# Performance work log

Hardware: AMD Instinct MI355X
Metric: run time of the kernel (lower is better)

The kernel has to match this reference:

```python
import jax, jax.numpy as jnp
import numpy as np

NUM_NODES = 50000
NUM_REL_ORIG = 5            # original relation types
NUM_REL = 2 * NUM_REL_ORIG + 1  # augmented: original + inverse + self-loop = 11
F_IN = 128
F_OUT = 128
NUM_EDGES = 800000


def setup_inputs() -> dict:
    key = jax.random.key(0)
    k1, k2, k3, k4, k5, k6 = jax.random.split(key, 6)
    src = jax.random.randint(k1, (NUM_EDGES,), 0, NUM_NODES, dtype=jnp.int32)
    rel = jax.random.randint(k2, (NUM_EDGES,), 0, NUM_REL_ORIG, dtype=jnp.int32)
    dst = jax.random.randint(k3, (NUM_EDGES,), 0, NUM_NODES, dtype=jnp.int32)
    graph = jnp.stack([src, rel, dst], axis=1)  # [E, 3] = (head, relation, tail)
    features = jax.random.normal(k4, (NUM_NODES, F_IN), dtype=jnp.float32)
    # RGCNConv parameters (no basis/block decomposition, bias=False, root_weight=True)
    glorot = lambda k, shape: jax.random.normal(k, shape, dtype=jnp.float32) * jnp.sqrt(2.0 / (shape[-2] + shape[-1]))
    weight = glorot(k5, (NUM_REL, F_IN, F_OUT))  # per-relation weights
    root = glorot(k6, (F_IN, F_OUT))             # root (self) weight
    return {"graph": graph, "features": features, "weight": weight, "root": root}


def reference(graph, features, weight, root):
    N = features.shape[0]
    R = weight.shape[0]
    n_orig = (R - 1) // 2
    src, rel, dst = graph[:, 0], graph[:, 1], graph[:, 2]
    loop = jnp.arange(N, dtype=graph.dtype)
    # augmented edge list: original, inverse, self-loops
    full_src = jnp.concatenate([src, dst, loop])
    full_dst = jnp.concatenate([dst, src, loop])
    full_rel = jnp.concatenate([rel, rel + n_orig, jnp.full((N,), 2 * n_orig, dtype=graph.dtype)])
    # per-(relation, dst-node) mean of source features (PyG RGCNConv aggr='mean'
    # aggregates raw x_j per relation, then applies W_r to the aggregate)
    seg = full_rel * N + full_dst  # [E_full]
    msgs = features[full_src]      # [E_full, F_in] gather
    sums = jax.ops.segment_sum(msgs, seg, num_segments=R * N)           # [R*N, F_in]
    cnts = jax.ops.segment_sum(jnp.ones((seg.shape[0],), features.dtype), seg, num_segments=R * N)
    mean = sums / jnp.maximum(cnts, 1.0)[:, None]
    mean = mean.reshape(R, N, -1)  # [R, N, F_in]
    # out = sum_r mean_r @ W_r + x @ W_root
    out = jnp.einsum('rnf,rfo->no', mean, weight) + features @ root
    return out
```

## Files before the change

### kernel.cpp

```cpp
#include <hip/hip_runtime.h>
#include <hip/hip_bf16.h>

#define NN 50000
#define RO 5
#define RT 11
#define FF 128
#define EE 800000
#define NBINS (2 * RO * NN)
#define SLOTS 32
#define FEAT_BLKS ((NN * FF / 4) / 256)
#define WT_BLKS ((RT * FF * FF) / 256)

typedef unsigned short u16;
typedef unsigned int u32;
typedef __attribute__((ext_vector_type(4))) unsigned short u16x4;
typedef __attribute__((ext_vector_type(4))) unsigned int u32x4;
typedef __attribute__((ext_vector_type(8))) short bf16x8;
typedef __attribute__((ext_vector_type(4))) float f32x4;

__device__ __forceinline__ u16 f2b(float x) {
  unsigned u = __float_as_uint(x);
  return (u16)((u + 0x7fffu + ((u >> 16) & 1u)) >> 16);
}

__global__ __launch_bounds__(256) void prep_k(const float* __restrict__ f,
                                              const float* __restrict__ w,
                                              const float* __restrict__ root,
                                              u16* __restrict__ fb,
                                              u16* __restrict__ wt) {
  int b = blockIdx.x;
  if (b < FEAT_BLKS) {
    int i = b * 256 + threadIdx.x;
    float4 v = reinterpret_cast<const float4*>(f)[i];
    u16x4 o;
    o.x = f2b(v.x); o.y = f2b(v.y); o.z = f2b(v.z); o.w = f2b(v.w);
    reinterpret_cast<u16x4*>(fb)[i] = o;
  } else if (b < FEAT_BLKS + WT_BLKS) {
    int idx = (b - FEAT_BLKS) * 256 + threadIdx.x;
    int r = idx >> 14;
    int rem = idx & 16383;
    int k = rem >> 7;
    int o = rem & 127;
    float v = w[idx];
    if (r == 10) v += root[rem];
    int chunk = (k >> 3) ^ (o & 7);
    wt[(r << 14) + (o << 7) + (chunk << 3) + (k & 7)] = f2b(v);
  } else {
    if (threadIdx.x < 64) reinterpret_cast<u32*>(fb)[NN * 64 + threadIdx.x] = 0;
  }
}

__global__ __launch_bounds__(256) void fill_k(const int* __restrict__ g,
                                              int* __restrict__ cur,
                                              u16* __restrict__ eidx) {
  const int e0 = (blockIdx.x * 256 + threadIdx.x) * 2;
  if (e0 >= EE) return;
  int s0 = g[3 * e0], r0 = g[3 * e0 + 1], d0 = g[3 * e0 + 2];
  int b0f = r0 * NN + d0;
  int b0r = (r0 + RO) * NN + s0;
  int p0f = atomicAdd(&cur[b0f], 1);
  int p0r = atomicAdd(&cur[b0r], 1);
  if (p0f < SLOTS) eidx[b0f * SLOTS + p0f] = (u16)s0;
  if (p0r < SLOTS) eidx[b0r * SLOTS + p0r] = (u16)d0;
  const int e1 = e0 + 1;
  if (e1 >= EE) return;
  int s1 = g[3 * e1], r1 = g[3 * e1 + 1], d1 = g[3 * e1 + 2];
  int b1f = r1 * NN + d1;
  int b1r = (r1 + RO) * NN + s1;
  int p1f = atomicAdd(&cur[b1f], 1);
  int p1r = atomicAdd(&cur[b1r], 1);
  if (p1f < SLOTS) eidx[b1f * SLOTS + p1f] = (u16)s1;
  if (p1r < SLOTS) eidx[b1r * SLOTS + p1r] = (u16)d1;
}

#define ACC(p) { a0 += __uint_as_float((p).x << 16); a1 += __uint_as_float((p).x & 0xffff0000u); \
                 a2 += __uint_as_float((p).y << 16); a3 += __uint_as_float((p).y & 0xffff0000u); \
                 a4 += __uint_as_float((p).z << 16); a5 += __uint_as_float((p).z & 0xffff0000u); \
                 a6 += __uint_as_float((p).w << 16); a7 += __uint_as_float((p).w & 0xffff0000u); }

__global__ __launch_bounds__(256) void mean_k(const int* __restrict__ cnt,
                                              const u32* __restrict__ eidx32,
                                              const u32x4* __restrict__ fv4,
                                              u32x4* __restrict__ Mv4) {
  const int lane = threadIdx.x & 63;
  const int wv   = threadIdx.x >> 6;
  const int q    = lane >> 4;
  const int l15  = lane & 15;
  const int q16  = q << 4;
  const int seg  = blockIdx.x * 16 + wv * 4 + q;
  const int c    = min(cnt[seg], SLOTS);
  const u32 slots = eidx32[seg * 16 + l15];

  int cmax = c;
  cmax = max(cmax, __shfl_xor(cmax, 16));
  cmax = max(cmax, __shfl_xor(cmax, 32));

  float a0 = 0.f, a1 = 0.f, a2 = 0.f, a3 = 0.f, a4 = 0.f, a5 = 0.f, a6 = 0.f, a7 = 0.f;

  for (int i = 0; i < cmax; i += 4) {
    u32 w0 = __shfl(slots, q16 + (i >> 1));
    u32 w1 = __shfl(slots, q16 + (i >> 1) + 1);
    int s0 = (i     < c) ? (int)(w0 & 0xffffu) : NN;
    int s1 = (i + 1 < c) ? (int)(w0 >> 16)     : NN;
    int s2 = (i + 2 < c) ? (int)(w1 & 0xffffu) : NN;
    int s3 = (i + 3 < c) ? (int)(w1 >> 16)     : NN;
    u32x4 p0 = fv4[s0 * 16 + l15];
    u32x4 p1 = fv4[s1 * 16 + l15];
    u32x4 p2 = fv4[s2 * 16 + l15];
    u32x4 p3 = fv4[s3 * 16 + l15];
    ACC(p0); ACC(p1); ACC(p2); ACC(p3);
  }

  const float inv = (c > 0) ? 1.0f / (float)c : 0.0f;
  u32x4 o;
  o.x = (u32)f2b(a0 * inv) | ((u32)f2b(a1 * inv) << 16);
  o.y = (u32)f2b(a2 * inv) | ((u32)f2b(a3 * inv) << 16);
  o.z = (u32)f2b(a4 * inv) | ((u32)f2b(a5 * inv) << 16);
  o.w = (u32)f2b(a6 * inv) | ((u32)f2b(a7 * inv) << 16);
  Mv4[seg * 16 + l15] = o;
}

__global__ __launch_bounds__(256) void gemm2_k(const u16* __restrict__ fbf,
                                               const u16* __restrict__ M,
                                               const u16* __restrict__ wt,
                                               float* __restrict__ out) {
  __shared__ __align__(16) u16 bs[128 * 128];
  const int tid  = threadIdx.x;
  const int lane = tid & 63;
  const int wv   = tid >> 6;
  const int l15  = lane & 15;
  const int ko   = lane >> 4;
  const int row  = blockIdx.x * 64 + wv * 16 + l15;
  const int rowc = (row < NN) ? row : 0;

  f32x4 acc[8];
#pragma unroll
  for (int i = 0; i < 8; ++i) acc[i] = (f32x4){0.f, 0.f, 0.f, 0.f};

  for (int r = 0; r < RT; ++r) {
    const bf16x8* wsrc = reinterpret_cast<const bf16x8*>(wt + (r << 14));
    bf16x8* ldst = reinterpret_cast<bf16x8*>(bs);
#pragma unroll
    for (int j = 0; j < 8; ++j) ldst[tid + j * 256] = wsrc[tid + j * 256];
    __syncthreads();

    const u16* arow = (r < 10) ? (M + ((long)r * NN + rowc) * FF)
                               : (fbf + (long)rowc * FF);
#pragma unroll
    for (int kc = 0; kc < 4; ++kc) {
      bf16x8 a = *reinterpret_cast<const bf16x8*>(arow + kc * 32 + ko * 8);
#pragma unroll
      for (int cf = 0; cf < 8; ++cf) {
        const int o = cf * 16 + l15;
        bf16x8 b = *reinterpret_cast<const bf16x8*>(
            &bs[(o << 7) + (((kc * 4 + ko) ^ (l15 & 7)) << 3)]);
        acc[cf] = __builtin_amdgcn_mfma_f32_16x16x32_bf16(a, b, acc[cf], 0, 0, 0);
      }
    }
    __syncthreads();
  }

  const int rbase = blockIdx.x * 64 + wv * 16 + ko * 4;
#pragma unroll
  for (int cf = 0; cf < 8; ++cf)
#pragma unroll
    for (int q2 = 0; q2 < 4; ++q2) {
      int rd = rbase + q2;
      if (rd < NN) out[rd * FF + cf * 16 + l15] = acc[cf][q2];
    }
}

extern "C" void kernel_launch(void* const* d_in, const int* in_sizes, int n_in,
                              void* d_out, int out_size, void* d_ws, size_t ws_size,
                              hipStream_t stream) {
  const int*   graph  = (const int*)d_in[0];
  const float* feat   = (const float*)d_in[1];
  const float* weight = (const float*)d_in[2];
  const float* root   = (const float*)d_in[3];
  float* out = (float*)d_out;
  char* ws = (char*)d_ws;

  u16* fbf  = (u16*)(ws);
  u16* wt   = (u16*)(ws + 12800512);
  int* cur  = (int*)(ws + 13160960);
  u16* eidx = (u16*)(ws + 15161088);
  u16* M    = (u16*)(ws + 47161088);

  hipMemsetAsync(cur, 0, NBINS * sizeof(int), stream);
  prep_k<<<FEAT_BLKS + WT_BLKS + 1, 256, 0, stream>>>(feat, weight, root, fbf, wt);
  fill_k<<<(EE / 2 + 255) / 256, 256, 0, stream>>>(graph, cur, eidx);
  mean_k<<<NBINS / 16, 256, 0, stream>>>(cur, (const u32*)eidx,
                                         (const u32x4*)fbf, (u32x4*)M);
  gemm2_k<<<(NN + 63) / 64, 256, 0, stream>>>(fbf, M, wt, out);
}
```

Measured before the change: 316.6 us.

## Fuse per-relation mean aggregation into GEMM, dropping intermediate mean buffer

Merges the mean-aggregation kernel and the GEMM kernel into one. Each block aggregates 32 destination nodes per relation into swizzled LDS and immediately multiplies the result by that relation's weight using MFMA. Weight fragments are read straight from global memory instead of being staged in LDS. This removes the write and re-read of the 10×N×128 bf16 mean tensor and one launch. In exchange, each block has less work per weight load, and an MFMA phase follows each gather with a barrier in between. The fill kernel also switches to one edge direction per thread for more parallelism.

```diff
diff --git a/kernel.cpp b/kernel.cpp
--- a/kernel.cpp
+++ b/kernel.cpp
@@ -6,8 +6,10 @@
 #define RT 11
 #define FF 128
 #define EE 800000
+#define EE2 (2 * EE)
 #define NBINS (2 * RO * NN)
 #define SLOTS 32
+#define DPB 32
 #define FEAT_BLKS ((NN * FF / 4) / 256)
 #define WT_BLKS ((RT * FF * FF) / 256)
 
@@ -53,121 +55,164 @@
 __global__ __launch_bounds__(256) void fill_k(const int* __restrict__ g,
                                               int* __restrict__ cur,
                                               u16* __restrict__ eidx) {
-  const int e0 = (blockIdx.x * 256 + threadIdx.x) * 2;
-  if (e0 >= EE) return;
-  int s0 = g[3 * e0], r0 = g[3 * e0 + 1], d0 = g[3 * e0 + 2];
-  int b0f = r0 * NN + d0;
-  int b0r = (r0 + RO) * NN + s0;
-  int p0f = atomicAdd(&cur[b0f], 1);
-  int p0r = atomicAdd(&cur[b0r], 1);
-  if (p0f < SLOTS) eidx[b0f * SLOTS + p0f] = (u16)s0;
-  if (p0r < SLOTS) eidx[b0r * SLOTS + p0r] = (u16)d0;
-  const int e1 = e0 + 1;
-  if (e1 >= EE) return;
-  int s1 = g[3 * e1], r1 = g[3 * e1 + 1], d1 = g[3 * e1 + 2];
-  int b1f = r1 * NN + d1;
-  int b1r = (r1 + RO) * NN + s1;
-  int p1f = atomicAdd(&cur[b1f], 1);
-  int p1r = atomicAdd(&cur[b1r], 1);
-  if (p1f < SLOTS) eidx[b1f * SLOTS + p1f] = (u16)s1;
-  if (p1r < SLOTS) eidx[b1r * SLOTS + p1r] = (u16)d1;
-}
-
-#define ACC(p) { a0 += __uint_as_float((p).x << 16); a1 += __uint_as_float((p).x & 0xffff0000u); \
-                 a2 += __uint_as_float((p).y << 16); a3 += __uint_as_float((p).y & 0xffff0000u); \
-                 a4 += __uint_as_float((p).z << 16); a5 += __uint_as_float((p).z & 0xffff0000u); \
-                 a6 += __uint_as_float((p).w << 16); a7 += __uint_as_float((p).w & 0xffff0000u); }
-
-__global__ __launch_bounds__(256) void mean_k(const int* __restrict__ cnt,
-                                              const u32* __restrict__ eidx32,
-                                              const u32x4* __restrict__ fv4,
-                                              u32x4* __restrict__ Mv4) {
-  const int lane = threadIdx.x & 63;
-  const int wv   = threadIdx.x >> 6;
-  const int q    = lane >> 4;
-  const int l15  = lane & 15;
-  const int q16  = q << 4;
-  const int seg  = blockIdx.x * 16 + wv * 4 + q;
-  const int c    = min(cnt[seg], SLOTS);
-  const u32 slots = eidx32[seg * 16 + l15];
-
-  int cmax = c;
-  cmax = max(cmax, __shfl_xor(cmax, 16));
-  cmax = max(cmax, __shfl_xor(cmax, 32));
-
-  float a0 = 0.f, a1 = 0.f, a2 = 0.f, a3 = 0.f, a4 = 0.f, a5 = 0.f, a6 = 0.f, a7 = 0.f;
-
-  for (int i = 0; i < cmax; i += 4) {
-    u32 w0 = __shfl(slots, q16 + (i >> 1));
-    u32 w1 = __shfl(slots, q16 + (i >> 1) + 1);
-    int s0 = (i     < c) ? (int)(w0 & 0xffffu) : NN;
-    int s1 = (i + 1 < c) ? (int)(w0 >> 16)     : NN;
-    int s2 = (i + 2 < c) ? (int)(w1 & 0xffffu) : NN;
-    int s3 = (i + 3 < c) ? (int)(w1 >> 16)     : NN;
-    u32x4 p0 = fv4[s0 * 16 + l15];
-    u32x4 p1 = fv4[s1 * 16 + l15];
-    u32x4 p2 = fv4[s2 * 16 + l15];
-    u32x4 p3 = fv4[s3 * 16 + l15];
-    ACC(p0); ACC(p1); ACC(p2); ACC(p3);
-  }
-
-  const float inv = (c > 0) ? 1.0f / (float)c : 0.0f;
-  u32x4 o;
-  o.x = (u32)f2b(a0 * inv) | ((u32)f2b(a1 * inv) << 16);
-  o.y = (u32)f2b(a2 * inv) | ((u32)f2b(a3 * inv) << 16);
-  o.z = (u32)f2b(a4 * inv) | ((u32)f2b(a5 * inv) << 16);
-  o.w = (u32)f2b(a6 * inv) | ((u32)f2b(a7 * inv) << 16);
-  Mv4[seg * 16 + l15] = o;
-}
-
-__global__ __launch_bounds__(256) void gemm2_k(const u16* __restrict__ fbf,
-                                               const u16* __restrict__ M,
-                                               const u16* __restrict__ wt,
-                                               float* __restrict__ out) {
-  __shared__ __align__(16) u16 bs[128 * 128];
+  const int m = blockIdx.x * 256 + threadIdx.x;
+  int e, bin; u16 val;
+  if (m < EE) {
+    e = m;
+    int s = g[3 * e], r = g[3 * e + 1], d = g[3 * e + 2];
+    bin = r * NN + d; val = (u16)s;
+  } else {
+    e = m - EE;
+    int d2 = g[3 * e], r = g[3 * e + 1], s2 = g[3 * e + 2];
+    bin = (r + RO) * NN + d2; val = (u16)s2;
+  }
+  int pos = atomicAdd(&cur[bin], 1);
+  if (pos < SLOTS) eidx[bin * SLOTS + pos] = val;
+}
+
+#define ACCX(p) { a0 += __uint_as_float((p).x << 16); a1 += __uint_as_float((p).x & 0xffff0000u); \
+                  a2 += __uint_as_float((p).y << 16); a3 += __uint_as_float((p).y & 0xffff0000u); \
+                  a4 += __uint_as_float((p).z << 16); a5 += __uint_as_float((p).z & 0xffff0000u); \
+                  a6 += __uint_as_float((p).w << 16); a7 += __uint_as_float((p).w & 0xffff0000u); }
+#define ACCY(p) { b0 += __uint_as_float((p).x << 16); b1 += __uint_as_float((p).x & 0xffff0000u); \
+                  b2 += __uint_as_float((p).y << 16); b3 += __uint_as_float((p).y & 0xffff0000u); \
+                  b4 += __uint_as_float((p).z << 16); b5 += __uint_as_float((p).z & 0xffff0000u); \
+                  b6 += __uint_as_float((p).w << 16); b7 += __uint_as_float((p).w & 0xffff0000u); }
+
+__global__ __launch_bounds__(256) void mg_k(const int* __restrict__ cnt,
+                                            const u32* __restrict__ eidx32,
+                                            const u32x4* __restrict__ fv4,
+                                            const u16* __restrict__ fbf,
+                                            const u16* __restrict__ wt,
+                                            float* __restrict__ out) {
+  __shared__ __align__(16) u32x4 Asw[DPB * 16];
   const int tid  = threadIdx.x;
   const int lane = tid & 63;
   const int wv   = tid >> 6;
   const int l15  = lane & 15;
   const int ko   = lane >> 4;
-  const int row  = blockIdx.x * 64 + wv * 16 + l15;
-  const int rowc = (row < NN) ? row : 0;
-
-  f32x4 acc[8];
-#pragma unroll
-  for (int i = 0; i < 8; ++i) acc[i] = (f32x4){0.f, 0.f, 0.f, 0.f};
-
-  for (int r = 0; r < RT; ++r) {
-    const bf16x8* wsrc = reinterpret_cast<const bf16x8*>(wt + (r << 14));
-    bf16x8* ldst = reinterpret_cast<bf16x8*>(bs);
-#pragma unroll
-    for (int j = 0; j < 8; ++j) ldst[tid + j * 256] = wsrc[tid + j * 256];
+  const int qid  = wv * 4 + ko;
+  const int q16  = ko << 4;
+  const int base = blockIdx.x * DPB;
+
+  f32x4 acc[2][2];
+#pragma unroll
+  for (int i = 0; i < 2; ++i)
+#pragma unroll
+    for (int j = 0; j < 2; ++j) acc[i][j] = (f32x4){0.f, 0.f, 0.f, 0.f};
+
+  const int row0 = qid * 2, row1 = row0 + 1;
+  const int d0 = base + row0, d1 = base + row1;
+  const bool v0 = d0 < NN, v1 = d1 < NN;
+
+  for (int r = 0; r < 10; ++r) {
+    const int seg0 = v0 ? r * NN + d0 : 0;
+    const int seg1 = v1 ? r * NN + d1 : 0;
+    const int c0 = v0 ? min(cnt[seg0], SLOTS) : 0;
+    const int c1 = v1 ? min(cnt[seg1], SLOTS) : 0;
+    const u32 sl0 = eidx32[seg0 * 16 + l15];
+    const u32 sl1 = eidx32[seg1 * 16 + l15];
+    int cmax = max(c0, c1);
+    cmax = max(cmax, __shfl_xor(cmax, 16));
+    cmax = max(cmax, __shfl_xor(cmax, 32));
+
+    float a0 = 0.f, a1 = 0.f, a2 = 0.f, a3 = 0.f, a4 = 0.f, a5 = 0.f, a6 = 0.f, a7 = 0.f;
+    float b0 = 0.f, b1 = 0.f, b2 = 0.f, b3 = 0.f, b4 = 0.f, b5 = 0.f, b6 = 0.f, b7 = 0.f;
+
+    for (int i = 0; i < cmax; i += 4) {
+      u32 wa0 = __shfl(sl0, q16 + (i >> 1));
+      u32 wa1 = __shfl(sl0, q16 + (i >> 1) + 1);
+      u32 wb0 = __shfl(sl1, q16 + (i >> 1));
+      u32 wb1 = __shfl(sl1, q16 + (i >> 1) + 1);
+      int s0 = (i     < c0) ? (int)(wa0 & 0xffffu) : NN;
+      int s1 = (i + 1 < c0) ? (int)(wa0 >> 16)     : NN;
+      int s2 = (i + 2 < c0) ? (int)(wa1 & 0xffffu) : NN;
+      int s3 = (i + 3 < c0) ? (int)(wa1 >> 16)     : NN;
+      int t0 = (i     < c1) ? (int)(wb0 & 0xffffu) : NN;
+      int t1 = (i + 1 < c1) ? (int)(wb0 >> 16)     : NN;
+      int t2 = (i + 2 < c1) ? (int)(wb1 & 0xffffu) : NN;
+      int t3 = (i + 3 < c1) ? (int)(wb1 >> 16)     : NN;
+      u32x4 p0 = fv4[s0 * 16 + l15];
+      u32x4 p1 = fv4[s1 * 16 + l15];
+      u32x4 p2 = fv4[s2 * 16 + l15];
+      u32x4 p3 = fv4[s3 * 16 + l15];
+      u32x4 p4 = fv4[t0 * 16 + l15];
+      u32x4 p5 = fv4[t1 * 16 + l15];
+      u32x4 p6 = fv4[t2 * 16 + l15];
+      u32x4 p7 = fv4[t3 * 16 + l15];
+      ACCX(p0); ACCX(p1); ACCX(p2); ACCX(p3);
+      ACCY(p4); ACCY(p5); ACCY(p6); ACCY(p7);
+    }
+
+    const float i0 = (c0 > 0) ? 1.0f / (float)c0 : 0.0f;
+    const float i1 = (c1 > 0) ? 1.0f / (float)c1 : 0.0f;
+    u32x4 m0, m1;
+    m0.x = (u32)f2b(a0 * i0) | ((u32)f2b(a1 * i0) << 16);
+    m0.y = (u32)f2b(a2 * i0) | ((u32)f2b(a3 * i0) << 16);
+    m0.z = (u32)f2b(a4 * i0) | ((u32)f2b(a5 * i0) << 16);
+    m0.w = (u32)f2b(a6 * i0) | ((u32)f2b(a7 * i0) << 16);
+    m1.x = (u32)f2b(b0 * i1) | ((u32)f2b(b1 * i1) << 16);
+    m1.y = (u32)f2b(b2 * i1) | ((u32)f2b(b3 * i1) << 16);
+    m1.z = (u32)f2b(b4 * i1) | ((u32)f2b(b5 * i1) << 16);
+    m1.w = (u32)f2b(b6 * i1) | ((u32)f2b(b7 * i1) << 16);
+    Asw[row0 * 16 + (l15 ^ (row0 & 7))] = m0;
+    Asw[row1 * 16 + (l15 ^ (row1 & 7))] = m1;
     __syncthreads();
 
-    const u16* arow = (r < 10) ? (M + ((long)r * NN + rowc) * FF)
-                               : (fbf + (long)rowc * FF);
+    const u16* wb = wt + (r << 14);
 #pragma unroll
     for (int kc = 0; kc < 4; ++kc) {
-      bf16x8 a = *reinterpret_cast<const bf16x8*>(arow + kc * 32 + ko * 8);
-#pragma unroll
-      for (int cf = 0; cf < 8; ++cf) {
-        const int o = cf * 16 + l15;
+      bf16x8 afr[2];
+#pragma unroll
+      for (int fq = 0; fq < 2; ++fq) {
+        const int arow = fq * 16 + l15;
+        afr[fq] = *reinterpret_cast<const bf16x8*>(
+            &Asw[arow * 16 + ((kc * 4 + ko) ^ (arow & 7))]);
+      }
+#pragma unroll
+      for (int fr = 0; fr < 2; ++fr) {
+        const int o = wv * 32 + fr * 16 + l15;
         bf16x8 b = *reinterpret_cast<const bf16x8*>(
-            &bs[(o << 7) + (((kc * 4 + ko) ^ (l15 & 7)) << 3)]);
-        acc[cf] = __builtin_amdgcn_mfma_f32_16x16x32_bf16(a, b, acc[cf], 0, 0, 0);
+            wb + (o << 7) + (((kc * 4 + ko) ^ (o & 7)) << 3));
+        acc[0][fr] = __builtin_amdgcn_mfma_f32_16x16x32_bf16(afr[0], b, acc[0][fr], 0, 0, 0);
+        acc[1][fr] = __builtin_amdgcn_mfma_f32_16x16x32_bf16(afr[1], b, acc[1][fr], 0, 0, 0);
       }
     }
     __syncthreads();
   }
 
-  const int rbase = blockIdx.x * 64 + wv * 16 + ko * 4;
-#pragma unroll
-  for (int cf = 0; cf < 8; ++cf)
-#pragma unroll
-    for (int q2 = 0; q2 < 4; ++q2) {
-      int rd = rbase + q2;
-      if (rd < NN) out[rd * FF + cf * 16 + l15] = acc[cf][q2];
+  {
+    const u16* wb = wt + (10 << 14);
+#pragma unroll
+    for (int kc = 0; kc < 4; ++kc) {
+      bf16x8 afr[2];
+#pragma unroll
+      for (int fq = 0; fq < 2; ++fq) {
+        int rowg = base + fq * 16 + l15;
+        rowg = (rowg < NN) ? rowg : NN;
+        afr[fq] = *reinterpret_cast<const bf16x8*>(
+            fbf + (long)rowg * FF + kc * 32 + ko * 8);
+      }
+#pragma unroll
+      for (int fr = 0; fr < 2; ++fr) {
+        const int o = wv * 32 + fr * 16 + l15;
+        bf16x8 b = *reinterpret_cast<const bf16x8*>(
+            wb + (o << 7) + (((kc * 4 + ko) ^ (o & 7)) << 3));
+        acc[0][fr] = __builtin_amdgcn_mfma_f32_16x16x32_bf16(afr[0], b, acc[0][fr], 0, 0, 0);
+        acc[1][fr] = __builtin_amdgcn_mfma_f32_16x16x32_bf16(afr[1], b, acc[1][fr], 0, 0, 0);
+      }
     }
+  }
+
+#pragma unroll
+  for (int fq = 0; fq < 2; ++fq)
+#pragma unroll
+    for (int fr = 0; fr < 2; ++fr)
+#pragma unroll
+      for (int q2 = 0; q2 < 4; ++q2) {
+        const int row = base + fq * 16 + ko * 4 + q2;
+        if (row < NN) out[row * FF + wv * 32 + fr * 16 + l15] = acc[fq][fr][q2];
+      }
 }
 
 extern "C" void kernel_launch(void* const* d_in, const int* in_sizes, int n_in,
@@ -184,12 +229,10 @@
   u16* wt   = (u16*)(ws + 12800512);
   int* cur  = (int*)(ws + 13160960);
   u16* eidx = (u16*)(ws + 15161088);
-  u16* M    = (u16*)(ws + 47161088);
 
   hipMemsetAsync(cur, 0, NBINS * sizeof(int), stream);
   prep_k<<<FEAT_BLKS + WT_BLKS + 1, 256, 0, stream>>>(feat, weight, root, fbf, wt);
-  fill_k<<<(EE / 2 + 255) / 256, 256, 0, stream>>>(graph, cur, eidx);
-  mean_k<<<NBINS / 16, 256, 0, stream>>>(cur, (const u32*)eidx,
-                                         (const u32x4*)fbf, (u32x4*)M);
-  gemm2_k<<<(NN + 63) / 64, 256, 0, stream>>>(fbf, M, wt, out);
-}
+  fill_k<<<EE2 / 256, 256, 0, stream>>>(graph, cur, eidx);
+  mg_k<<<(NN + DPB - 1) / DPB, 256, 0, stream>>>(cur, (const u32*)eidx,
+                                                 (const u32x4*)fbf, fbf, wt, out);
+}
```

Measured after the change: 288.1 us. -9.0%, faster.
